# Performance work log

Hardware: AMD Instinct MI355X
Metric: run time of the kernel (lower is better)

The kernel has to match this reference:

```python
import jax, jax.numpy as jnp
import numpy as np

DIM = 1024
HEADS = 16
HEAD_DIM = DIM // HEADS
B, N = 4, 4096


def setup_inputs() -> dict:
    key = jax.random.key(0)
    ks = jax.random.split(key, 10)
    s = 1.0 / np.sqrt(DIM)
    return {
        "x": jax.random.normal(ks[0], (B, N, DIM), dtype=jnp.float32),
        "Wq": jax.random.uniform(ks[1], (DIM, DIM), jnp.float32, -s, s),
        "bq": jax.random.uniform(ks[2], (DIM,), jnp.float32, -s, s),
        "Wk": jax.random.uniform(ks[3], (DIM, DIM), jnp.float32, -s, s),
        "bk": jax.random.uniform(ks[4], (DIM,), jnp.float32, -s, s),
        "Wv": jax.random.uniform(ks[5], (DIM, DIM), jnp.float32, -s, s),
        "bv": jax.random.uniform(ks[6], (DIM,), jnp.float32, -s, s),
        "Wo": jax.random.uniform(ks[7], (DIM, DIM), jnp.float32, -s, s),
        "bo": jax.random.uniform(ks[8], (DIM,), jnp.float32, -s, s),
        "stdp": jnp.ones((HEADS,), dtype=jnp.float32),
    }


def reference(x, Wq, bq, Wk, bk, Wv, bv, Wo, bo, stdp):
    b, n, d = x.shape
    h, dh = HEADS, HEAD_DIM
    # projections (torch Linear: x @ W.T + b)
    def proj(W, bias):
        return (x @ W.T + bias).reshape(b, n, h, dh).transpose(0, 2, 1, 3)  # bhnd
    Q = jax.nn.elu(proj(Wq, bq)) + 1.0
    K = jax.nn.elu(proj(Wk, bk)) + 1.0
    V = proj(Wv, bv)
    stdp_w = jax.nn.sigmoid(stdp).reshape(1, h, 1, 1)
    KV = jnp.einsum('bhnd,bhnv->bhdv', K, V)      # (b,h,dh,dh)
    K_sum = K.sum(axis=2)                          # (b,h,dh)
    numerator = jnp.einsum('bhnd,bhdv->bhnv', Q, KV)
    denominator = jnp.einsum('bhnd,bhd->bhn', Q, K_sum)[..., None] + 1e-6
    attn_out = numerator / denominator * stdp_w    # (b,h,n,dh)
    out = attn_out.transpose(0, 2, 1, 3).reshape(b, n, d)
    out = out @ Wo.T + bo
    return (out, jax.lax.stop_gradient(stdp))
```

## Files before the change

### kernel.cpp

```cpp
#include <hip/hip_runtime.h>
#include <hip/hip_bf16.h>

#define DIMSZ 1024
#define SEQLEN 4096
#define NHEAD 16
#define NX 16777216L
#define NW 1048576L
#define KVSPLITS 8

typedef __attribute__((ext_vector_type(8))) short bf16x8;
typedef __attribute__((ext_vector_type(4))) float f32x4;

__device__ __forceinline__ unsigned short f2bf(float f) {
    union { float f; unsigned int i; } c; c.f = f;
    unsigned int x = c.i;
    unsigned int r = (x + 0x7fffu + ((x >> 16) & 1u)) >> 16;
    return (unsigned short)r;
}

__device__ __forceinline__ unsigned int pk2(float lo, float hi) {
    union { float f; unsigned int i; } a, b; a.f = lo; b.f = hi;
    return __builtin_amdgcn_perm(b.i + 0x8000u, a.i + 0x8000u, 0x07060302u);
}

__device__ __forceinline__ void unp8r(bf16x8 v, float* f) {
    union { bf16x8 s; uint4 w; } u; u.s = v;
    union { unsigned int i; float f; } c;
    c.i = u.w.x << 16;           f[0] = c.f;
    c.i = u.w.x & 0xffff0000u;   f[1] = c.f;
    c.i = u.w.y << 16;           f[2] = c.f;
    c.i = u.w.y & 0xffff0000u;   f[3] = c.f;
    c.i = u.w.z << 16;           f[4] = c.f;
    c.i = u.w.z & 0xffff0000u;   f[5] = c.f;
    c.i = u.w.w << 16;           f[6] = c.f;
    c.i = u.w.w & 0xffff0000u;   f[7] = c.f;
}

__device__ __forceinline__ void async16(const void* g, void* l) {
    __builtin_amdgcn_global_load_lds(
        (const __attribute__((address_space(1))) void*)g,
        (__attribute__((address_space(3))) void*)l,
        16, 0, 0);
}

__global__ __launch_bounds__(256) void cast_pack(
    const float* __restrict__ x, const float* __restrict__ Wq,
    const float* __restrict__ Wk, const float* __restrict__ Wv,
    const float* __restrict__ Wo, const float* __restrict__ stdp,
    unsigned short* __restrict__ xb, unsigned short* __restrict__ Wqkv,
    unsigned short* __restrict__ Wob, float* __restrict__ outTail)
{
    long i4 = ((long)blockIdx.x * 256 + threadIdx.x) * 4;
    const float* src; unsigned short* dst; long off;
    if (i4 < NX)               { src = x;  dst = xb;          off = i4; }
    else if (i4 < NX + NW)     { src = Wq; dst = Wqkv;        off = i4 - NX; }
    else if (i4 < NX + 2*NW)   { src = Wk; dst = Wqkv + NW;   off = i4 - NX - NW; }
    else if (i4 < NX + 3*NW)   { src = Wv; dst = Wqkv + 2*NW; off = i4 - NX - 2*NW; }
    else                       { src = Wo; dst = Wob;         off = i4 - NX - 3*NW; }
    float4 v = *(const float4*)(src + off);
    union { unsigned short u[4]; uint2 p; } o;
    o.u[0] = f2bf(v.x); o.u[1] = f2bf(v.y); o.u[2] = f2bf(v.z); o.u[3] = f2bf(v.w);
    *(uint2*)(dst + off) = o.p;
    if (blockIdx.x == 0 && threadIdx.x < NHEAD) outTail[threadIdx.x] = stdp[threadIdx.x];
}

__global__ __launch_bounds__(512, 2) void qkv_gemm8(
    const unsigned short* __restrict__ A, const unsigned short* __restrict__ W,
    const float* __restrict__ bq, const float* __restrict__ bk,
    const float* __restrict__ bv,
    unsigned short* __restrict__ Qb, unsigned short* __restrict__ Kb,
    unsigned short* __restrict__ Vb)
{
    __shared__ __align__(16) char SM[131072];
    const int t = threadIdx.x;
    const int wave = t >> 6, lane = t & 63;
    const int lr = lane & 15, lq = lane >> 4;
    const int wm = wave >> 2, wn = wave & 3;
    const int m0 = blockIdx.x * 256;
    const int c0 = blockIdx.y * 256;

    const int sc = (((t & 7) ^ ((t >> 3) & 7)) * 8);
    const unsigned short* pA = A + (long)(m0 + (t >> 3)) * DIMSZ + sc;
    const unsigned short* pB = W + (long)(c0 + (t >> 3)) * DIMSZ + sc;
    char* ldsW = SM + wave * 1024;

    const int xo = ((lq ^ (lr & 7)) << 4);
    const char* ABase = SM + wm * 16384 + lr * 128;
    const char* BBase = SM + 32768 + (wn * 64 + lr) * 128;

    f32x4 acc[8][4];
    #pragma unroll
    for (int i = 0; i < 8; ++i)
        #pragma unroll
        for (int j = 0; j < 4; ++j) acc[i][j] = (f32x4){0.f, 0.f, 0.f, 0.f};

#define STAGE(Q, O) do {                                                        \
        if ((Q) < 16) {                                                         \
            const int isB_ = ((O) < 2) ? 1 : 0;                                 \
            const int half_ = isB_ ? (O) : ((O) - 2);                           \
            const unsigned short* s_ = (isB_ ? pB : pA)                         \
                                       + (long)half_ * 131072 + (Q) * 64;       \
            char* d_ = ldsW + (((Q) & 1) << 16) + isB_ * 32768 + half_ * 16384; \
            async16(s_, d_);                                                    \
            async16(s_ + 65536, d_ + 8192);                                     \
        }                                                                       \
    } while (0)

    STAGE(0, 0); STAGE(0, 1); STAGE(0, 2); STAGE(0, 3);
    STAGE(1, 0); STAGE(1, 1); STAGE(1, 2);
    asm volatile("s_waitcnt vmcnt(6)" ::: "memory");
    __builtin_amdgcn_s_barrier();

    for (int kt = 0; kt < 16; ++kt) {
        const int buf = (kt & 1) << 16;
        bf16x8 a0[4][2], a1[4][2], bfr[4][2];

        #pragma unroll
        for (int j = 0; j < 4; ++j) {
            bfr[j][0] = *(const bf16x8*)(BBase + buf + j * 2048 + xo);
            bfr[j][1] = *(const bf16x8*)(BBase + buf + j * 2048 + (xo ^ 64));
        }
        #pragma unroll
        for (int i = 0; i < 4; ++i) {
            a0[i][0] = *(const bf16x8*)(ABase + buf + i * 2048 + xo);
            a0[i][1] = *(const bf16x8*)(ABase + buf + i * 2048 + (xo ^ 64));
        }
        STAGE(kt + 1, 3);
        asm volatile("s_waitcnt lgkmcnt(8)" ::: "memory");
        __builtin_amdgcn_s_barrier();
        asm volatile("s_waitcnt lgkmcnt(0)" ::: "memory");
        __builtin_amdgcn_sched_barrier(0);
        __builtin_amdgcn_s_setprio(1);
        #pragma unroll
        for (int s = 0; s < 2; ++s)
            #pragma unroll
            for (int i = 0; i < 4; ++i)
                #pragma unroll
                for (int j = 0; j < 2; ++j)
                    acc[i][j] = __builtin_amdgcn_mfma_f32_16x16x32_bf16(
                        bfr[j][s], a0[i][s], acc[i][j], 0, 0, 0);
        __builtin_amdgcn_s_setprio(0);
        __builtin_amdgcn_s_barrier();

        STAGE(kt + 2, 0);
        __builtin_amdgcn_s_barrier();
        __builtin_amdgcn_s_setprio(1);
        #pragma unroll
        for (int s = 0; s < 2; ++s)
            #pragma unroll
            for (int i = 0; i < 4; ++i)
                #pragma unroll
                for (int j = 2; j < 4; ++j)
                    acc[i][j] = __builtin_amdgcn_mfma_f32_16x16x32_bf16(
                        bfr[j][s], a0[i][s], acc[i][j], 0, 0, 0);
        __builtin_amdgcn_s_setprio(0);
        __builtin_amdgcn_s_barrier();

        #pragma unroll
        for (int i = 0; i < 4; ++i) {
            a1[i][0] = *(const bf16x8*)(ABase + buf + (i + 4) * 2048 + xo);
            a1[i][1] = *(const bf16x8*)(ABase + buf + (i + 4) * 2048 + (xo ^ 64));
        }
        STAGE(kt + 2, 1);
        __builtin_amdgcn_s_barrier();
        asm volatile("s_waitcnt lgkmcnt(0)" ::: "memory");
        __builtin_amdgcn_sched_barrier(0);
        __builtin_amdgcn_s_setprio(1);
        #pragma unroll
        for (int s = 0; s < 2; ++s)
            #pragma unroll
            for (int i = 0; i < 4; ++i)
                #pragma unroll
                for (int j = 0; j < 2; ++j)
                    acc[i + 4][j] = __builtin_amdgcn_mfma_f32_16x16x32_bf16(
                        bfr[j][s], a1[i][s], acc[i + 4][j], 0, 0, 0);
        __builtin_amdgcn_s_setprio(0);
        __builtin_amdgcn_s_barrier();

        STAGE(kt + 2, 2);
        __builtin_amdgcn_s_barrier();
        __builtin_amdgcn_s_setprio(1);
        #pragma unroll
        for (int s = 0; s < 2; ++s)
            #pragma unroll
            for (int i = 0; i < 4; ++i)
                #pragma unroll
                for (int j = 2; j < 4; ++j)
                    acc[i + 4][j] = __builtin_amdgcn_mfma_f32_16x16x32_bf16(
                        bfr[j][s], a1[i][s], acc[i + 4][j], 0, 0, 0);
        __builtin_amdgcn_s_setprio(0);
        if (kt < 14)       asm volatile("s_waitcnt vmcnt(6)" ::: "memory");
        else if (kt == 14) asm volatile("s_waitcnt vmcnt(0)" ::: "memory");
        __builtin_amdgcn_s_barrier();
    }
#undef STAGE

    const int proj = c0 >> 10;
    const float* bias = proj == 0 ? bq : (proj == 1 ? bk : bv);
    const bool qk = proj < 2;
    const int cb = (c0 & 1023) + wn * 64;
    const int q4 = lq * 4;
    #pragma unroll
    for (int j = 0; j < 4; ++j) {
        const float4 b4 = *(const float4*)(bias + cb + 16 * j + q4);
        #pragma unroll
        for (int i = 0; i < 8; ++i) {
            float v0 = acc[i][j][0] + b4.x, v1 = acc[i][j][1] + b4.y;
            float v2 = acc[i][j][2] + b4.z, v3 = acc[i][j][3] + b4.w;
            if (qk) {
                v0 = v0 > 0.f ? v0 + 1.f : __expf(v0);
                v1 = v1 > 0.f ? v1 + 1.f : __expf(v1);
                v2 = v2 > 0.f ? v2 + 1.f : __expf(v2);
                v3 = v3 > 0.f ? v3 + 1.f : __expf(v3);
            }
            const int row = wm * 128 + 16 * i + lr;
            int byte = row * 512 + wn * 128 + j * 32 + q4 * 2;
            byte ^= (row & 7) << 4;
            uint2 pkd; pkd.x = pk2(v0, v1); pkd.y = pk2(v2, v3);
            *(uint2*)(SM + byte) = pkd;
        }
    }
    __syncthreads();
    unsigned short* dstp = proj == 0 ? Qb : (proj == 1 ? Kb : Vb);
    const int colsh = (t & 31) * 8;
    const int h = ((c0 >> 6) + (colsh >> 6)) & 15;
    const int b_ = m0 >> 12;
    unsigned short* dbase = dstp + ((long)(b_ * 16 + h) * SEQLEN) * 64 + (colsh & 63);
    #pragma unroll
    for (int u = 0; u < 16; ++u) {
        const int flat = u * 8192 + t * 16;
        const int row = flat >> 9;
        uint4 val = *(const uint4*)(SM + (flat ^ ((row & 7) << 4)));
        const int n = (m0 + row) & 4095;
        *(uint4*)(dbase + (long)n * 64) = val;
    }
}

__global__ __launch_bounds__(256) void kv_reduce(
    const unsigned short* __restrict__ Kb, const unsigned short* __restrict__ Vb,
    float* __restrict__ KVp, float* __restrict__ Ksump)
{
    __shared__ __align__(16) char LDS[65536];
    int bh = blockIdx.x, split = blockIdx.y, t = threadIdx.x;
    int wave = t >> 6, lane = t & 63, lr = lane & 15, lq = lane >> 4;

    const int nl = t & 127;
    const int dh = (t >> 7) * 32;
    const int vrow = 16 * wave + lr;

    f32x4 acc[4];
    #pragma unroll
    for (int j = 0; j < 4; ++j) acc[j] = (f32x4){0.f, 0.f, 0.f, 0.f};
    float ksp[4] = {0.f, 0.f, 0.f, 0.f};

    for (int half = 0; half < 2; ++half) {
        const unsigned short* Kbase = Kb + ((long)bh * SEQLEN + split * 512 + half * 256) * 64;
        const unsigned short* Vbase = Vb + ((long)bh * SEQLEN + split * 512 + half * 256) * 64;

        union Q2S { uint4 q[4]; unsigned short s[32]; };
        Q2S kq[2], vq[2];
        #pragma unroll
        for (int it = 0; it < 2; ++it) {
            const unsigned short* kp = Kbase + (long)(it * 128 + nl) * 64 + dh;
            const unsigned short* vp = Vbase + (long)(it * 128 + nl) * 64 + dh;
            #pragma unroll
            for (int g = 0; g < 4; ++g) {
                kq[it].q[g] = *(const uint4*)(kp + g * 8);
                vq[it].q[g] = *(const uint4*)(vp + g * 8);
            }
        }
        if (half) __syncthreads();
        #pragma unroll
        for (int it = 0; it < 2; ++it) {
            char* buf = LDS + it * 32768;
            #pragma unroll
            for (int e = 0; e < 32; ++e) {
                const int d = dh + e;
                const int a = d * 256 + ((nl * 2) ^ ((d & 7) << 4));
                *(unsigned short*)(buf + a) = kq[it].s[e];
                *(unsigned short*)(buf + 16384 + a) = vq[it].s[e];
            }
        }
        __syncthreads();

        #pragma unroll
        for (int it = 0; it < 2; ++it) {
            const char* buf = LDS + it * 32768;
            #pragma unroll
            for (int ns = 0; ns < 4; ++ns) {
                const int xoff = (ns * 64 + lq * 16) ^ ((lr & 7) << 4);
                bf16x8 af = *(const bf16x8*)(buf + 16384 + vrow * 256 + xoff);
                bf16x8 bfr[4];
                #pragma unroll
                for (int j = 0; j < 4; ++j)
                    bfr[j] = *(const bf16x8*)(buf + (16 * j + lr) * 256 + xoff);
                if (wave == 0) {
                    #pragma unroll
                    for (int j = 0; j < 4; ++j) {
                        float kf[8]; unp8r(bfr[j], kf);
                        ksp[j] += ((kf[0] + kf[1]) + (kf[2] + kf[3]))
                                + ((kf[4] + kf[5]) + (kf[6] + kf[7]));
                    }
                }
                #pragma unroll
                for (int j = 0; j < 4; ++j)
                    acc[j] = __builtin_amdgcn_mfma_f32_16x16x32_bf16(bfr[j], af, acc[j], 0, 0, 0);
            }
        }
    }

    float* kp = KVp + ((long)split * 64 + bh) * 4096;
    const int q4 = lq * 4;
    #pragma unroll
    for (int j = 0; j < 4; ++j)
        *(f32x4*)(kp + vrow * 64 + 16 * j + q4) = acc[j];

    if (wave == 0) {
        #pragma unroll
        for (int j = 0; j < 4; ++j) {
            float s = ksp[j];
            s += __shfl_xor(s, 16);
            s += __shfl_xor(s, 32);
            if (lane < 16)
                Ksump[((long)split * 64 + bh) * 64 + 16 * j + lr] = s;
        }
    }
}

__global__ __launch_bounds__(256) void kv_final(
    const float* __restrict__ KVp, const float* __restrict__ Ksump,
    unsigned short* __restrict__ KVb, float* __restrict__ Ksum)
{
    int bh = blockIdx.x, t = threadIdx.x;
    float s[16];
    #pragma unroll
    for (int g = 0; g < 16; ++g) s[g] = 0.f;
    for (int sp = 0; sp < KVSPLITS; ++sp) {
        const float* src = KVp + ((long)sp * 64 + bh) * 4096 + t * 16;
        #pragma unroll
        for (int g = 0; g < 4; ++g) {
            float4 v = *(const float4*)(src + g * 4);
            s[g * 4 + 0] += v.x; s[g * 4 + 1] += v.y;
            s[g * 4 + 2] += v.z; s[g * 4 + 3] += v.w;
        }
    }
    uint4 o0, o1;
    o0.x = pk2(s[0], s[1]);  o0.y = pk2(s[2], s[3]);
    o0.z = pk2(s[4], s[5]);  o0.w = pk2(s[6], s[7]);
    o1.x = pk2(s[8], s[9]);  o1.y = pk2(s[10], s[11]);
    o1.z = pk2(s[12], s[13]); o1.w = pk2(s[14], s[15]);
    *(uint4*)(KVb + (long)bh * 4096 + t * 16) = o0;
    *(uint4*)(KVb + (long)bh * 4096 + t * 16 + 8) = o1;
    if (t < 16) {
        float4 a = {0.f, 0.f, 0.f, 0.f};
        for (int p = 0; p < KVSPLITS; p += 4) {
            #pragma unroll
            for (int q = 0; q < 4; ++q) {
                float4 v = *(const float4*)(Ksump + ((long)(p + q) * 64 + bh) * 64 + t * 4);
                a.x += v.x; a.y += v.y; a.z += v.z; a.w += v.w;
            }
        }
        *(float4*)(Ksum + bh * 64 + t * 4) = a;
    }
}

__global__ __launch_bounds__(256) void attn_kernel(
    const unsigned short* __restrict__ Qb, const unsigned short* __restrict__ KVb,
    const float* __restrict__ Ksum, const float* __restrict__ stdp,
    unsigned short* __restrict__ attn)
{
    __shared__ unsigned short Cs[256 * 72];
    int t = threadIdx.x;
    int bh = blockIdx.y;
    int b = bh >> 4, h = bh & 15;

    int wave = t >> 6, lane = t & 63, lr = lane & 15, lk = (lane >> 4) * 8;
    const unsigned short* kvb = KVb + (long)bh * 4096;
    const float* ksb = Ksum + bh * 64;

    bf16x8 bfrh[2][4];
    float ksf[2][8];
    #pragma unroll
    for (int s = 0; s < 2; ++s) {
        #pragma unroll
        for (int j = 0; j < 4; ++j)
            bfrh[s][j] = *(const bf16x8*)(kvb + (16 * j + lr) * 64 + s * 32 + lk);
        float4 ka = *(const float4*)(ksb + s * 32 + lk);
        float4 kb2 = *(const float4*)(ksb + s * 32 + lk + 4);
        ksf[s][0] = ka.x; ksf[s][1] = ka.y; ksf[s][2] = ka.z; ksf[s][3] = ka.w;
        ksf[s][4] = kb2.x; ksf[s][5] = kb2.y; ksf[s][6] = kb2.z; ksf[s][7] = kb2.w;
    }
    float sg = 1.f / (1.f + __expf(-stdp[h]));
    int q4 = (lane >> 4) * 4;

    for (int c = 0; c < 2; ++c) {
        int rc = blockIdx.x * 2 + c;
        int rowbase = rc * 256 + wave * 64;

        f32x4 acc[4][4];
        #pragma unroll
        for (int i = 0; i < 4; ++i)
            #pragma unroll
            for (int j = 0; j < 4; ++j) acc[i][j] = (f32x4){0.f, 0.f, 0.f, 0.f};
        float ds[4] = {0.f, 0.f, 0.f, 0.f};

        #pragma unroll
        for (int s = 0; s < 2; ++s) {
            bf16x8 af[4];
            #pragma unroll
            for (int i = 0; i < 4; ++i)
                af[i] = *(const bf16x8*)(Qb + ((long)bh * SEQLEN + rowbase + 16 * i + lr) * 64 + s * 32 + lk);
            #pragma unroll
            for (int i = 0; i < 4; ++i) {
                float qf[8]; unp8r(af[i], qf);
                #pragma unroll
                for (int e = 0; e < 8; ++e) ds[i] += qf[e] * ksf[s][e];
            }
            #pragma unroll
            for (int i = 0; i < 4; ++i)
                #pragma unroll
                for (int j = 0; j < 4; ++j)
                    acc[i][j] = __builtin_amdgcn_mfma_f32_16x16x32_bf16(bfrh[s][j], af[i], acc[i][j], 0, 0, 0);
        }

        float dinv_i[4];
        #pragma unroll
        for (int i = 0; i < 4; ++i) {
            float d = ds[i];
            d += __shfl_xor(d, 16);
            d += __shfl_xor(d, 32);
            dinv_i[i] = sg / (d + 1e-6f);
        }

        #pragma unroll
        for (int j = 0; j < 4; ++j) {
            int v0c = 16 * j + q4;
            #pragma unroll
            for (int i = 0; i < 4; ++i) {
                int row = wave * 64 + 16 * i + lr;
                float d = dinv_i[i];
                uint2 pkd;
                pkd.x = pk2(acc[i][j][0] * d, acc[i][j][1] * d);
                pkd.y = pk2(acc[i][j][2] * d, acc[i][j][3] * d);
                *(uint2*)(Cs + row * 72 + v0c) = pkd;
            }
        }
        __syncthreads();
        #pragma unroll
        for (int u = 0; u < 8; ++u) {
            int row = u * 32 + (t >> 3);
            int nn = rc * 256 + row;
            long a = ((long)(b * SEQLEN + nn)) * DIMSZ + h * 64 + (t & 7) * 8;
            *(uint4*)(attn + a) = *(const uint4*)(Cs + row * 72 + (t & 7) * 8);
        }
        __syncthreads();
    }
}

__global__ __launch_bounds__(512, 2) void out_gemm8(
    const unsigned short* __restrict__ A, const unsigned short* __restrict__ W,
    const float* __restrict__ bo, float* __restrict__ out)
{
    __shared__ __align__(16) char SM[131072];
    const int t = threadIdx.x;
    const int wave = t >> 6, lane = t & 63;
    const int lr = lane & 15, lq = lane >> 4;
    const int wm = wave >> 2, wn = wave & 3;
    const int m0 = blockIdx.x * 256;
    const int c0 = blockIdx.y * 256;

    const int sc = (((t & 7) ^ ((t >> 3) & 7)) * 8);
    const unsigned short* pA = A + (long)(m0 + (t >> 3)) * DIMSZ + sc;
    const unsigned short* pB = W + (long)(c0 + (t >> 3)) * DIMSZ + sc;
    char* ldsW = SM + wave * 1024;

    const int xo = ((lq ^ (lr & 7)) << 4);
    const char* ABase = SM + wm * 16384 + lr * 128;
    const char* BBase = SM + 32768 + (wn * 64 + lr) * 128;

    f32x4 acc[8][4];
    #pragma unroll
    for (int i = 0; i < 8; ++i)
        #pragma unroll
        for (int j = 0; j < 4; ++j) acc[i][j] = (f32x4){0.f, 0.f, 0.f, 0.f};

#define STAGE(Q, O) do {                                                        \
        if ((Q) < 16) {                                                         \
            const int isB_ = ((O) < 2) ? 1 : 0;                                 \
            const int half_ = isB_ ? (O) : ((O) - 2);                           \
            const unsigned short* s_ = (isB_ ? pB : pA)                         \
                                       + (long)half_ * 131072 + (Q) * 64;       \
            char* d_ = ldsW + (((Q) & 1) << 16) + isB_ * 32768 + half_ * 16384; \
            async16(s_, d_);                                                    \
            async16(s_ + 65536, d_ + 8192);                                     \
        }                                                                       \
    } while (0)

    STAGE(0, 0); STAGE(0, 1); STAGE(0, 2); STAGE(0, 3);
    STAGE(1, 0); STAGE(1, 1); STAGE(1, 2);
    asm volatile("s_waitcnt vmcnt(6)" ::: "memory");
    __builtin_amdgcn_s_barrier();

    for (int kt = 0; kt < 16; ++kt) {
        const int buf = (kt & 1) << 16;
        bf16x8 a0[4][2], a1[4][2], bfr[4][2];

        #pragma unroll
        for (int j = 0; j < 4; ++j) {
            bfr[j][0] = *(const bf16x8*)(BBase + buf + j * 2048 + xo);
            bfr[j][1] = *(const bf16x8*)(BBase + buf + j * 2048 + (xo ^ 64));
        }
        #pragma unroll
        for (int i = 0; i < 4; ++i) {
            a0[i][0] = *(const bf16x8*)(ABase + buf + i * 2048 + xo);
            a0[i][1] = *(const bf16x8*)(ABase + buf + i * 2048 + (xo ^ 64));
        }
        STAGE(kt + 1, 3);
        asm volatile("s_waitcnt lgkmcnt(8)" ::: "memory");
        __builtin_amdgcn_s_barrier();
        asm volatile("s_waitcnt lgkmcnt(0)" ::: "memory");
        __builtin_amdgcn_sched_barrier(0);
        __builtin_amdgcn_s_setprio(1);
        #pragma unroll
        for (int s = 0; s < 2; ++s)
            #pragma unroll
            for (int i = 0; i < 4; ++i)
                #pragma unroll
                for (int j = 0; j < 2; ++j)
                    acc[i][j] = __builtin_amdgcn_mfma_f32_16x16x32_bf16(
                        bfr[j][s], a0[i][s], acc[i][j], 0, 0, 0);
        __builtin_amdgcn_s_setprio(0);
        __builtin_amdgcn_s_barrier();

        STAGE(kt + 2, 0);
        __builtin_amdgcn_s_barrier();
        __builtin_amdgcn_s_setprio(1);
        #pragma unroll
        for (int s = 0; s < 2; ++s)
            #pragma unroll
            for (int i = 0; i < 4; ++i)
                #pragma unroll
                for (int j = 2; j < 4; ++j)
                    acc[i][j] = __builtin_amdgcn_mfma_f32_16x16x32_bf16(
                        bfr[j][s], a0[i][s], acc[i][j], 0, 0, 0);
        __builtin_amdgcn_s_setprio(0);
        __builtin_amdgcn_s_barrier();

        #pragma unroll
        for (int i = 0; i < 4; ++i) {
            a1[i][0] = *(const bf16x8*)(ABase + buf + (i + 4) * 2048 + xo);
            a1[i][1] = *(const bf16x8*)(ABase + buf + (i + 4) * 2048 + (xo ^ 64));
        }
        STAGE(kt + 2, 1);
        __builtin_amdgcn_s_barrier();
        asm volatile("s_waitcnt lgkmcnt(0)" ::: "memory");
        __builtin_amdgcn_sched_barrier(0);
        __builtin_amdgcn_s_setprio(1);
        #pragma unroll
        for (int s = 0; s < 2; ++s)
            #pragma unroll
            for (int i = 0; i < 4; ++i)
                #pragma unroll
                for (int j = 0; j < 2; ++j)
                    acc[i + 4][j] = __builtin_amdgcn_mfma_f32_16x16x32_bf16(
                        bfr[j][s], a1[i][s], acc[i + 4][j], 0, 0, 0);
        __builtin_amdgcn_s_setprio(0);
        __builtin_amdgcn_s_barrier();

        STAGE(kt + 2, 2);
        __builtin_amdgcn_s_barrier();
        __builtin_amdgcn_s_setprio(1);
        #pragma unroll
        for (int s = 0; s < 2; ++s)
            #pragma unroll
            for (int i = 0; i < 4; ++i)
                #pragma unroll
                for (int j = 2; j < 4; ++j)
                    acc[i + 4][j] = __builtin_amdgcn_mfma_f32_16x16x32_bf16(
                        bfr[j][s], a1[i][s], acc[i + 4][j], 0, 0, 0);
        __builtin_amdgcn_s_setprio(0);
        if (kt < 14)       asm volatile("s_waitcnt vmcnt(6)" ::: "memory");
        else if (kt == 14) asm volatile("s_waitcnt vmcnt(0)" ::: "memory");
        __builtin_amdgcn_s_barrier();
    }
#undef STAGE

    const int q4 = lq * 4;
    #pragma unroll
    for (int j = 0; j < 4; ++j) {
        const int c = c0 + wn * 64 + 16 * j + q4;
        const float4 b4 = *(const float4*)(bo + c);
        #pragma unroll
        for (int i = 0; i < 8; ++i) {
            const int gm = m0 + wm * 128 + 16 * i + lr;
            float4 v;
            v.x = acc[i][j][0] + b4.x; v.y = acc[i][j][1] + b4.y;
            v.z = acc[i][j][2] + b4.z; v.w = acc[i][j][3] + b4.w;
            *(float4*)(out + (long)gm * DIMSZ + c) = v;
        }
    }
}

extern "C" void kernel_launch(void* const* d_in, const int* in_sizes, int n_in,
                              void* d_out, int out_size, void* d_ws, size_t ws_size,
                              hipStream_t stream) {
    const float* x    = (const float*)d_in[0];
    const float* Wq   = (const float*)d_in[1];
    const float* bq   = (const float*)d_in[2];
    const float* Wk   = (const float*)d_in[3];
    const float* bk   = (const float*)d_in[4];
    const float* Wv   = (const float*)d_in[5];
    const float* bv   = (const float*)d_in[6];
    const float* Wo   = (const float*)d_in[7];
    const float* bo   = (const float*)d_in[8];
    const float* stdp = (const float*)d_in[9];
    float* out = (float*)d_out;

    char* ws = (char*)d_ws;
    unsigned short* xb   = (unsigned short*)(ws);
    float*          KVp  = (float*)(ws);
    unsigned short* attn = (unsigned short*)(ws);
    unsigned short* Wqkv = (unsigned short*)(ws + 33554432L);
    float*          Ksump= (float*)(ws + 33554432L);
    unsigned short* KVb  = (unsigned short*)(ws + 33816576L);
    float*          Ksum = (float*)(ws + 34340864L);
    unsigned short* Wob  = (unsigned short*)(ws + 39845888L);
    unsigned short* Qb   = (unsigned short*)(ws + 41943040L);
    unsigned short* Kb   = (unsigned short*)(ws + 75497472L);
    unsigned short* Vb   = (unsigned short*)(ws + 109051904L);

    cast_pack<<<20480, 256, 0, stream>>>(x, Wq, Wk, Wv, Wo, stdp, xb, Wqkv, Wob,
                                         out + 16777216L);
    qkv_gemm8<<<dim3(64, 12), 512, 0, stream>>>(xb, Wqkv, bq, bk, bv, Qb, Kb, Vb);
    kv_reduce<<<dim3(64, KVSPLITS), 256, 0, stream>>>(Kb, Vb, KVp, Ksump);
    kv_final<<<64, 256, 0, stream>>>(KVp, Ksump, KVb, Ksum);
    attn_kernel<<<dim3(8, 64), 256, 0, stream>>>(Qb, KVb, Ksum, stdp, attn);
    out_gemm8<<<dim3(64, 4), 512, 0, stream>>>(attn, Wob, bo, out);
}
```

Before: 325.8 us.

## Hoist all LDS fragment reads to loop top and batch staging to cut barriers

Both GEMM main loops now issue every LDS fragment read for the k-tile (all B and both A halves) up front. The MFMA quadrants are then gated by graded lgkmcnt waits instead of barrier pairs. The three async global-to-LDS stage copies for tile kt+2 are grouped after a single barrier before the last MFMA quadrant, which removes several workgroup barriers per iteration. This trades higher register pressure and less interleaving of global copies with compute for fewer synchronisation stalls. Correctness depends on the lgkmcnt counts matching the number of outstanding LDS reads, and on the kt+2 stage writes not overlapping buffers that are still being read.

```diff
diff --git a/kernel.cpp b/kernel.cpp
--- a/kernel.cpp
+++ b/kernel.cpp
@@ -116,7 +116,7 @@
         bf16x8 a0[4][2], a1[4][2], bfr[4][2];
 
         #pragma unroll
-        for (int j = 0; j < 4; ++j) {
+        for (int j = 0; j < 2; ++j) {
             bfr[j][0] = *(const bf16x8*)(BBase + buf + j * 2048 + xo);
             bfr[j][1] = *(const bf16x8*)(BBase + buf + j * 2048 + (xo ^ 64));
         }
@@ -125,10 +125,22 @@
             a0[i][0] = *(const bf16x8*)(ABase + buf + i * 2048 + xo);
             a0[i][1] = *(const bf16x8*)(ABase + buf + i * 2048 + (xo ^ 64));
         }
+        __builtin_amdgcn_sched_barrier(0);
+        #pragma unroll
+        for (int j = 2; j < 4; ++j) {
+            bfr[j][0] = *(const bf16x8*)(BBase + buf + j * 2048 + xo);
+            bfr[j][1] = *(const bf16x8*)(BBase + buf + j * 2048 + (xo ^ 64));
+        }
+        __builtin_amdgcn_sched_barrier(0);
+        #pragma unroll
+        for (int i = 0; i < 4; ++i) {
+            a1[i][0] = *(const bf16x8*)(ABase + buf + (i + 4) * 2048 + xo);
+            a1[i][1] = *(const bf16x8*)(ABase + buf + (i + 4) * 2048 + (xo ^ 64));
+        }
+        __builtin_amdgcn_sched_barrier(0);
         STAGE(kt + 1, 3);
-        asm volatile("s_waitcnt lgkmcnt(8)" ::: "memory");
-        __builtin_amdgcn_s_barrier();
-        asm volatile("s_waitcnt lgkmcnt(0)" ::: "memory");
+
+        asm volatile("s_waitcnt lgkmcnt(12)" ::: "memory");
         __builtin_amdgcn_sched_barrier(0);
         __builtin_amdgcn_s_setprio(1);
         #pragma unroll
@@ -140,10 +152,9 @@
                     acc[i][j] = __builtin_amdgcn_mfma_f32_16x16x32_bf16(
                         bfr[j][s], a0[i][s], acc[i][j], 0, 0, 0);
         __builtin_amdgcn_s_setprio(0);
-        __builtin_amdgcn_s_barrier();
-
-        STAGE(kt + 2, 0);
-        __builtin_amdgcn_s_barrier();
+
+        asm volatile("s_waitcnt lgkmcnt(8)" ::: "memory");
+        __builtin_amdgcn_sched_barrier(0);
         __builtin_amdgcn_s_setprio(1);
         #pragma unroll
         for (int s = 0; s < 2; ++s)
@@ -154,15 +165,7 @@
                     acc[i][j] = __builtin_amdgcn_mfma_f32_16x16x32_bf16(
                         bfr[j][s], a0[i][s], acc[i][j], 0, 0, 0);
         __builtin_amdgcn_s_setprio(0);
-        __builtin_amdgcn_s_barrier();
-
-        #pragma unroll
-        for (int i = 0; i < 4; ++i) {
-            a1[i][0] = *(const bf16x8*)(ABase + buf + (i + 4) * 2048 + xo);
-            a1[i][1] = *(const bf16x8*)(ABase + buf + (i + 4) * 2048 + (xo ^ 64));
-        }
-        STAGE(kt + 2, 1);
-        __builtin_amdgcn_s_barrier();
+
         asm volatile("s_waitcnt lgkmcnt(0)" ::: "memory");
         __builtin_amdgcn_sched_barrier(0);
         __builtin_amdgcn_s_setprio(1);
@@ -175,10 +178,10 @@
                     acc[i + 4][j] = __builtin_amdgcn_mfma_f32_16x16x32_bf16(
                         bfr[j][s], a1[i][s], acc[i + 4][j], 0, 0, 0);
         __builtin_amdgcn_s_setprio(0);
+
         __builtin_amdgcn_s_barrier();
-
-        STAGE(kt + 2, 2);
-        __builtin_amdgcn_s_barrier();
+        STAGE(kt + 2, 0); STAGE(kt + 2, 1); STAGE(kt + 2, 2);
+
         __builtin_amdgcn_s_setprio(1);
         #pragma unroll
         for (int s = 0; s < 2; ++s)
@@ -189,6 +192,7 @@
                     acc[i + 4][j] = __builtin_amdgcn_mfma_f32_16x16x32_bf16(
                         bfr[j][s], a1[i][s], acc[i + 4][j], 0, 0, 0);
         __builtin_amdgcn_s_setprio(0);
+
         if (kt < 14)       asm volatile("s_waitcnt vmcnt(6)" ::: "memory");
         else if (kt == 14) asm volatile("s_waitcnt vmcnt(0)" ::: "memory");
         __builtin_amdgcn_s_barrier();
@@ -506,7 +510,7 @@
         bf16x8 a0[4][2], a1[4][2], bfr[4][2];
 
         #pragma unroll
-        for (int j = 0; j < 4; ++j) {
+        for (int j = 0; j < 2; ++j) {
             bfr[j][0] = *(const bf16x8*)(BBase + buf + j * 2048 + xo);
             bfr[j][1] = *(const bf16x8*)(BBase + buf + j * 2048 + (xo ^ 64));
         }
@@ -515,10 +519,22 @@
             a0[i][0] = *(const bf16x8*)(ABase + buf + i * 2048 + xo);
             a0[i][1] = *(const bf16x8*)(ABase + buf + i * 2048 + (xo ^ 64));
         }
+        __builtin_amdgcn_sched_barrier(0);
+        #pragma unroll
+        for (int j = 2; j < 4; ++j) {
+            bfr[j][0] = *(const bf16x8*)(BBase + buf + j * 2048 + xo);
+            bfr[j][1] = *(const bf16x8*)(BBase + buf + j * 2048 + (xo ^ 64));
+        }
+        __builtin_amdgcn_sched_barrier(0);
+        #pragma unroll
+        for (int i = 0; i < 4; ++i) {
+            a1[i][0] = *(const bf16x8*)(ABase + buf + (i + 4) * 2048 + xo);
+            a1[i][1] = *(const bf16x8*)(ABase + buf + (i + 4) * 2048 + (xo ^ 64));
+        }
+        __builtin_amdgcn_sched_barrier(0);
         STAGE(kt + 1, 3);
-        asm volatile("s_waitcnt lgkmcnt(8)" ::: "memory");
-        __builtin_amdgcn_s_barrier();
-        asm volatile("s_waitcnt lgkmcnt(0)" ::: "memory");
+
+        asm volatile("s_waitcnt lgkmcnt(12)" ::: "memory");
         __builtin_amdgcn_sched_barrier(0);
         __builtin_amdgcn_s_setprio(1);
         #pragma unroll
@@ -530,10 +546,9 @@
                     acc[i][j] = __builtin_amdgcn_mfma_f32_16x16x32_bf16(
                         bfr[j][s], a0[i][s], acc[i][j], 0, 0, 0);
         __builtin_amdgcn_s_setprio(0);
-        __builtin_amdgcn_s_barrier();
-
-        STAGE(kt + 2, 0);
-        __builtin_amdgcn_s_barrier();
+
+        asm volatile("s_waitcnt lgkmcnt(8)" ::: "memory");
+        __builtin_amdgcn_sched_barrier(0);
         __builtin_amdgcn_s_setprio(1);
         #pragma unroll
         for (int s = 0; s < 2; ++s)
@@ -544,15 +559,7 @@
                     acc[i][j] = __builtin_amdgcn_mfma_f32_16x16x32_bf16(
                         bfr[j][s], a0[i][s], acc[i][j], 0, 0, 0);
         __builtin_amdgcn_s_setprio(0);
-        __builtin_amdgcn_s_barrier();
-
-        #pragma unroll
-        for (int i = 0; i < 4; ++i) {
-            a1[i][0] = *(const bf16x8*)(ABase + buf + (i + 4) * 2048 + xo);
-            a1[i][1] = *(const bf16x8*)(ABase + buf + (i + 4) * 2048 + (xo ^ 64));
-        }
-        STAGE(kt + 2, 1);
-        __builtin_amdgcn_s_barrier();
+
         asm volatile("s_waitcnt lgkmcnt(0)" ::: "memory");
         __builtin_amdgcn_sched_barrier(0);
         __builtin_amdgcn_s_setprio(1);
@@ -565,10 +572,10 @@
                     acc[i + 4][j] = __builtin_amdgcn_mfma_f32_16x16x32_bf16(
                         bfr[j][s], a1[i][s], acc[i + 4][j], 0, 0, 0);
         __builtin_amdgcn_s_setprio(0);
+
         __builtin_amdgcn_s_barrier();
-
-        STAGE(kt + 2, 2);
-        __builtin_amdgcn_s_barrier();
+        STAGE(kt + 2, 0); STAGE(kt + 2, 1); STAGE(kt + 2, 2);
+
         __builtin_amdgcn_s_setprio(1);
         #pragma unroll
         for (int s = 0; s < 2; ++s)
@@ -579,6 +586,7 @@
                     acc[i + 4][j] = __builtin_amdgcn_mfma_f32_16x16x32_bf16(
                         bfr[j][s], a1[i][s], acc[i + 4][j], 0, 0, 0);
         __builtin_amdgcn_s_setprio(0);
+
         if (kt < 14)       asm volatile("s_waitcnt vmcnt(6)" ::: "memory");
         else if (kt == 14) asm volatile("s_waitcnt vmcnt(0)" ::: "memory");
         __builtin_amdgcn_s_barrier();
```

Result: faster. 315.4 us (-3.2%).
